# Optimization experiments

Hardware: AMD Instinct MI355X
Metric: run time of the kernel (lower is better)

The kernel has to match this reference:

```python
import jax, jax.numpy as jnp
import numpy as np
from jax import lax

T, D_IN, D_OUT = 8192, 4096, 4096
N_ADAPT, RANK = 8, 16


def setup_inputs() -> dict:
    key = jax.random.key(0)
    ks = jax.random.split(key, 6)
    x = jax.random.normal(ks[0], (T, D_IN), jnp.float32)
    weight_indices = jax.random.randint(ks[1], (T,), 0, N_ADAPT, jnp.int64 if jax.config.jax_enable_x64 else jnp.int32)
    W_base = jax.random.normal(ks[2], (D_OUT, D_IN), jnp.float32) * 0.02
    A_buffer = jax.random.normal(ks[3], (N_ADAPT, D_IN, RANK), jnp.float32) * 0.02
    B_buffer = jax.random.normal(ks[4], (N_ADAPT, RANK, D_OUT), jnp.float32) * 0.02
    DeltaW = jax.random.normal(ks[5], (N_ADAPT, D_IN, D_OUT), jnp.float32) * 0.02
    return {"x": x, "weight_indices": weight_indices, "W_base": W_base,
            "A_buffer": A_buffer, "B_buffer": B_buffer, "DeltaW": DeltaW}


def _ldmm(indices, x, A, B, D):
    """Per-token adapter matmul: out[t] = x[t] @ (DeltaW[j] + A[j] @ B[j]), j = indices[t].
    Grouped by adapter via masked GEMMs (fixed small adapter count), jit-friendly."""
    n_adapt = A.shape[0]
    acc0 = jnp.zeros((x.shape[0], D.shape[2]), x.dtype)

    def body(acc, inp):
        a_id, A_a, B_a, D_a = inp
        mask = (indices == a_id)[:, None]
        xm = jnp.where(mask, x, jnp.zeros((), x.dtype))  # [T, in]
        W_eff = D_a + A_a @ B_a                          # [in, out]
        return acc + xm @ W_eff, None

    acc, _ = lax.scan(body, acc0, (jnp.arange(n_adapt), A, B, D))
    return acc


def reference(x, weight_indices, W_base, A_buffer, B_buffer, DeltaW):
    base = x @ W_base.T                                   # ColumnParallelLinear
    delta = _ldmm(weight_indices, x, A_buffer, B_buffer, DeltaW)
    # NOTE: source has `base_output = +output` (unary plus, likely a typo for `+=`);
    # we implement the intended fused semantics base + ldmm.
    return base + delta
```

## Files before the change

### kernel.cpp

```cpp
#include <hip/hip_runtime.h>


#define T_TOKENS 8192
#define DIM 4096
#define NADAPT 8
#define RANK 16

#define BM2 256
#define MAXT2 40
#define GRIDX2 (MAXT2 * 16)

#define BM1 128
#define MAXT1 72

typedef __attribute__((ext_vector_type(8))) short bf16x8;
typedef __attribute__((ext_vector_type(4))) float f32x4;

__device__ __forceinline__ unsigned short f2bf(float f) {
  union { float f; unsigned u; } v; v.f = f;
  unsigned r = v.u + 0x7FFFu + ((v.u >> 16) & 1u);
  return (unsigned short)(r >> 16);
}

__device__ __forceinline__ void gload_lds16(const void* g, void* l) {
  __builtin_amdgcn_global_load_lds(
      (const __attribute__((address_space(1))) void*)g,
      (__attribute__((address_space(3))) void*)l, 16, 0, 0);
}

template <int N> __device__ __forceinline__ void vmwait() {
  if constexpr (N == 0)      asm volatile("s_waitcnt vmcnt(0)" ::: "memory");
  else if constexpr (N == 4) asm volatile("s_waitcnt vmcnt(4)" ::: "memory");
  else if constexpr (N == 8) asm volatile("s_waitcnt vmcnt(8)" ::: "memory");
}

__global__ void prep_kernel(const int* __restrict__ idx, int* __restrict__ perm,
                            int* __restrict__ meta, int padm) {
  __shared__ int s_cnt[NADAPT];
  __shared__ int s_padoff[NADAPT + 1];
  __shared__ int s_wsum[16];
  const int tid = threadIdx.x;
  const int lane = tid & 63;
  const int wave = tid >> 6;

  if (tid < NADAPT) s_cnt[tid] = 0;
  __syncthreads();
  for (int t = tid; t < T_TOKENS; t += 1024) atomicAdd(&s_cnt[idx[t]], 1);
  __syncthreads();

  if (tid == 0) {
    int off = 0, nt = 0;
    for (int j = 0; j < NADAPT; ++j) {
      meta[j] = s_cnt[j];
      s_padoff[j] = off;
      const int c = s_cnt[j];
      const int ntj = (c + padm - 1) / padm;
      for (int i = 0; i < ntj; ++i) {
        meta[32 + 3 * nt + 0] = j;
        meta[32 + 3 * nt + 1] = off + i * padm;
        meta[32 + 3 * nt + 2] = min(padm, c - i * padm);
        ++nt;
      }
      off += ntj * padm;
    }
    s_padoff[NADAPT] = off;
    meta[17] = nt;
    for (int j = 0; j <= NADAPT; ++j) meta[8 + j] = s_padoff[j];
  }
  __syncthreads();

  const int total_pad = s_padoff[NADAPT];
  for (int t = tid; t < total_pad; t += 1024) perm[t] = -1;
  __syncthreads();

  for (int j = 0; j < NADAPT; ++j) {
    int base = s_padoff[j];
    for (int c0 = 0; c0 < T_TOKENS; c0 += 1024) {
      const int t = c0 + tid;
      const int flag = (idx[t] == j) ? 1 : 0;
      const unsigned long long bal = __ballot(flag);
      const int wpos = __popcll(bal & ((1ULL << lane) - 1ULL));
      if (lane == 0) s_wsum[wave] = __popcll(bal);
      __syncthreads();
      int woff = 0, ctot = 0;
      for (int w = 0; w < 16; ++w) {
        const int v = s_wsum[w];
        if (w < wave) woff += v;
        ctot += v;
      }
      if (flag) perm[base + woff + wpos] = t;
      base += ctot;
      __syncthreads();
    }
  }
}

__global__ void convert_x_kernel(const float* __restrict__ x,
                                 unsigned short* __restrict__ xb) {
  const long long i = (long long)blockIdx.x * 256 + threadIdx.x;
  const float4* x4 = (const float4*)x;
  const float4 a = x4[2 * i];
  const float4 b = x4[2 * i + 1];
  uint4 o;
  o.x = (unsigned)f2bf(a.x) | ((unsigned)f2bf(a.y) << 16);
  o.y = (unsigned)f2bf(a.z) | ((unsigned)f2bf(a.w) << 16);
  o.z = (unsigned)f2bf(b.x) | ((unsigned)f2bf(b.y) << 16);
  o.w = (unsigned)f2bf(b.z) | ((unsigned)f2bf(b.w) << 16);
  ((uint4*)xb)[i] = o;
}

__global__ __launch_bounds__(256) void build_wtot_kernel(
    const float* __restrict__ Wb, const float* __restrict__ Am,
    const float* __restrict__ Bm, const float* __restrict__ DW,
    unsigned short* __restrict__ Wt, int j0) {
  const int jj = blockIdx.z;
  const int j = j0 + jj;
  const int i0 = blockIdx.x << 6;
  const int o0 = blockIdx.y << 6;
  __shared__ float Dl[64 * 64];
  __shared__ float Alt[16][68];
  __shared__ float Bl[16][68];
  const int tid = threadIdx.x;

  const float* dwp = DW + ((size_t)j * DIM + i0) * DIM + o0;
#pragma unroll
  for (int q = 0; q < 4; ++q) {
    const int lin = q * 256 + tid;
    const int i = lin >> 4;
    const int o4 = (lin & 15) << 2;
    const float4 v = *(const float4*)(dwp + (size_t)i * DIM + o4);
    const int iq = i >> 2, ie = i & 3;
#pragma unroll
    for (int k = 0; k < 4; ++k) {
      const int o = o4 + k;
      Dl[o * 64 + (((iq ^ (o & 15)) << 2) | ie)] = ((const float*)&v)[k];
    }
  }
  {
    const int ai = tid >> 2, r4 = (tid & 3) << 2;
    const float4 v = *(const float4*)(Am + ((size_t)j * DIM + i0 + ai) * RANK + r4);
#pragma unroll
    for (int k = 0; k < 4; ++k) Alt[r4 + k][ai] = ((const float*)&v)[k];
  }
  {
    const int br = tid >> 4, bo4 = (tid & 15) << 2;
    const float4 v = *(const float4*)(Bm + ((size_t)j * RANK + br) * DIM + o0 + bo4);
    *(float4*)&Bl[br][bo4] = v;
  }
  __syncthreads();

  const int to = (tid >> 4) << 2;
  const int ti = (tid & 15) << 2;
  float acc[4][4];

#pragma unroll
  for (int m = 0; m < 4; ++m) {
    const int o = to + m;
    const float4 w = *(const float4*)(Wb + (size_t)(o0 + o) * DIM + i0 + ti);
    const float4 d = *(const float4*)&Dl[o * 64 + (((ti >> 2) ^ (o & 15)) << 2)];
    acc[m][0] = w.x + d.x; acc[m][1] = w.y + d.y;
    acc[m][2] = w.z + d.z; acc[m][3] = w.w + d.w;
  }
#pragma unroll
  for (int r = 0; r < RANK; ++r) {
    const float4 av = *(const float4*)&Alt[r][ti];
    const float4 bv = *(const float4*)&Bl[r][to];
#pragma unroll
    for (int m = 0; m < 4; ++m) {
      const float b = ((const float*)&bv)[m];
      acc[m][0] += b * av.x; acc[m][1] += b * av.y;
      acc[m][2] += b * av.z; acc[m][3] += b * av.w;
    }
  }
#pragma unroll
  for (int m = 0; m < 4; ++m) {
    const int o = to + m;
    const unsigned lo = (unsigned)f2bf(acc[m][0]) | ((unsigned)f2bf(acc[m][1]) << 16);
    const unsigned hi = (unsigned)f2bf(acc[m][2]) | ((unsigned)f2bf(acc[m][3]) << 16);
    uint2 pk; pk.x = lo; pk.y = hi;
    *(uint2*)(Wt + ((size_t)jj * DIM + o0 + o) * DIM + i0 + ti) = pk;
  }
}

template <int BUF, int KK, int MQ, int VME, int SGRP, int SOP, int SKH, bool DOST>
__device__ __forceinline__ void do_phase(
    char* smem, int tid, int stile,
    const unsigned short* const* aB, const unsigned short* const* bB,
    const int* aoff, const int* boff, bf16x8* bfr, f32x4 (*acc)[4]) {
  const int grp = (BUF * 2 + KK) * 16384;
  if constexpr (MQ == 0) {
#pragma unroll
    for (int n = 0; n < 4; ++n)
      bfr[n] = *(const bf16x8*)(smem + 65536 + grp + boff[n]);
  }
  bf16x8 afr[4];
#pragma unroll
  for (int i = 0; i < 4; ++i)
    afr[i] = *(const bf16x8*)(smem + grp + aoff[MQ * 4 + i]);
  if constexpr (DOST) {
    const unsigned short* const* bs = SOP ? bB : aB;
#pragma unroll
    for (int q = 0; q < 2; ++q)
      gload_lds16(bs[q] + stile * 64 + SKH * 32,
                  smem + SOP * 65536 + SGRP * 16384 + q * 8192 + tid * 16);
  }
  __builtin_amdgcn_s_barrier();
  asm volatile("s_waitcnt lgkmcnt(0)" ::: "memory");
  __builtin_amdgcn_s_setprio(1);
#pragma unroll
  for (int i = 0; i < 4; ++i)
#pragma unroll
    for (int n = 0; n < 4; ++n)
      acc[MQ * 4 + i][n] =
          __builtin_amdgcn_mfma_f32_16x16x32_bf16(afr[i], bfr[n], acc[MQ * 4 + i][n], 0, 0, 0);
  __builtin_amdgcn_s_setprio(0);
  vmwait<VME>();
  __builtin_amdgcn_s_barrier();
}

template <int SGRP, int SOP, int SKH>
__device__ __forceinline__ void do_stage(
    char* smem, int tid, int stile,
    const unsigned short* const* aB, const unsigned short* const* bB) {
  const unsigned short* const* bs = SOP ? bB : aB;
#pragma unroll
  for (int q = 0; q < 2; ++q)
    gload_lds16(bs[q] + stile * 64 + SKH * 32,
                smem + SOP * 65536 + SGRP * 16384 + q * 8192 + tid * 16);
}

__global__ __launch_bounds__(512, 2) void gemm8_kernel(
    const unsigned short* __restrict__ xb, const unsigned short* __restrict__ Wt,
    const int* __restrict__ perm, const int* __restrict__ meta,
    float* __restrict__ out, int j0, int npp) {
  extern __shared__ char smem[];
  const int ntiles = meta[17];
  const int flat = blockIdx.x;
  const int swz = (flat & 7) * (GRIDX2 / 8) + (flat >> 3);
  const int mt = swz >> 4;
  const int nt = swz & 15;
  if (mt >= ntiles) return;
  const int adapter = meta[32 + 3 * mt];
  if (adapter < j0 || adapter >= j0 + npp) return;
  const int slot = adapter - j0;
  const int pbase = meta[32 + 3 * mt + 1];
  const int nbase = nt << 8;

  const int tid = threadIdx.x;
  const int lane = tid & 63;
  const int wave = tid >> 6;
  const int wr = wave >> 2, wc = wave & 3;
  const int fr = lane & 15, kg = lane >> 4;

  int aoff[8], boff[4];
#pragma unroll
  for (int m = 0; m < 8; ++m) {
    const int row = wr * 128 + m * 16 + fr;
    const int r = row >> 1, hf = row & 1;
    const int c = ((hf << 2) | kg) ^ (r & 7);
    aoff[m] = r * 128 + c * 16;
  }
#pragma unroll
  for (int n = 0; n < 4; ++n) {
    const int row = wc * 64 + n * 16 + fr;
    const int r = row >> 1, hf = row & 1;
    const int c = ((hf << 2) | kg) ^ (r & 7);
    boff[n] = r * 128 + c * 16;
  }

  const unsigned short* aB[2];
  const unsigned short* bB[2];
#pragma unroll
  for (int q = 0; q < 2; ++q) {
    const int L = q * 512 + tid;
    const int r = L >> 3, c = L & 7;
    const int s = c ^ (r & 7);
    const int grow = 2 * r + (s >> 2);
    const int gk = (s & 3) << 3;
    int pr = perm[pbase + grow];
    if (pr < 0) pr = 0;
    aB[q] = xb + (size_t)pr * DIM + gk;
    bB[q] = Wt + ((size_t)slot * DIM + nbase + grow) * DIM + gk;
  }

  const f32x4 zero = {0.f, 0.f, 0.f, 0.f};
  f32x4 acc[8][4];
#pragma unroll
  for (int m = 0; m < 8; ++m)
#pragma unroll
    for (int n = 0; n < 4; ++n) acc[m][n] = zero;
  bf16x8 bfr[4];

  do_stage<0, 0, 0>(smem, tid, 0, aB, bB);
  do_stage<0, 1, 0>(smem, tid, 0, aB, bB);
  do_stage<1, 0, 1>(smem, tid, 0, aB, bB);
  do_stage<1, 1, 1>(smem, tid, 0, aB, bB);
  do_stage<2, 0, 0>(smem, tid, 1, aB, bB);
  do_stage<2, 1, 0>(smem, tid, 1, aB, bB);
  vmwait<8>();
  __builtin_amdgcn_s_barrier();

  for (int it = 0; it < 31; ++it) {
    const int t1 = 2 * it + 1, t2 = 2 * it + 2, t3 = 2 * it + 3;
    do_phase<0, 0, 0, -1, 3, 0, 1, true>(smem, tid, t1, aB, bB, aoff, boff, bfr, acc);
    do_phase<0, 0, 1,  8, 3, 1, 1, true>(smem, tid, t1, aB, bB, aoff, boff, bfr, acc);
    do_phase<0, 1, 0, -1, 0, 0, 0, true>(smem, tid, t2, aB, bB, aoff, boff, bfr, acc);
    do_phase<0, 1, 1,  8, 0, 1, 0, true>(smem, tid, t2, aB, bB, aoff, boff, bfr, acc);
    do_phase<1, 0, 0, -1, 1, 0, 1, true>(smem, tid, t2, aB, bB, aoff, boff, bfr, acc);
    do_phase<1, 0, 1,  8, 1, 1, 1, true>(smem, tid, t2, aB, bB, aoff, boff, bfr, acc);
    do_phase<1, 1, 0, -1, 2, 0, 0, true>(smem, tid, t3, aB, bB, aoff, boff, bfr, acc);
    do_phase<1, 1, 1,  8, 2, 1, 0, true>(smem, tid, t3, aB, bB, aoff, boff, bfr, acc);
  }
  do_phase<0, 0, 0, -1, 3, 0, 1, true >(smem, tid, 63, aB, bB, aoff, boff, bfr, acc);
  do_phase<0, 0, 1,  8, 3, 1, 1, true >(smem, tid, 63, aB, bB, aoff, boff, bfr, acc);
  do_phase<0, 1, 0, -1, 0, 0, 0, false>(smem, tid, 0,  aB, bB, aoff, boff, bfr, acc);
  do_phase<0, 1, 1,  4, 0, 0, 0, false>(smem, tid, 0,  aB, bB, aoff, boff, bfr, acc);
  do_phase<1, 0, 0, -1, 0, 0, 0, false>(smem, tid, 0,  aB, bB, aoff, boff, bfr, acc);
  do_phase<1, 0, 1,  0, 0, 0, 0, false>(smem, tid, 0,  aB, bB, aoff, boff, bfr, acc);
  do_phase<1, 1, 0, -1, 0, 0, 0, false>(smem, tid, 0,  aB, bB, aoff, boff, bfr, acc);
  do_phase<1, 1, 1, -1, 0, 0, 0, false>(smem, tid, 0,  aB, bB, aoff, boff, bfr, acc);

#pragma unroll
  for (int m = 0; m < 8; ++m) {
#pragma unroll
    for (int t = 0; t < 4; ++t) {
      const int rt = wr * 128 + m * 16 + kg * 4 + t;
      const int pr = perm[pbase + rt];
      if (pr < 0) continue;
      float* orow = out + (size_t)pr * DIM + nbase + wc * 64;
#pragma unroll
      for (int n = 0; n < 4; ++n) orow[n * 16 + fr] = acc[m][n][t];
    }
  }
}

template <bool USE_XB>
__global__ __launch_bounds__(256) void gemm_kernel(
    const unsigned short* __restrict__ xb, const float* __restrict__ xf,
    const unsigned short* __restrict__ Wt,
    const int* __restrict__ perm, const int* __restrict__ meta,
    float* __restrict__ out, int j0, int npp) {
  const int ntiles = meta[17];
  const int mt = blockIdx.x;
  if (mt >= ntiles) return;
  const int adapter = meta[32 + 3 * mt];
  if (adapter < j0 || adapter >= j0 + npp) return;
  const int slot = adapter - j0;
  const int nt = blockIdx.y;
  const int pbase = meta[32 + 3 * mt + 1];
  const int nbase = nt << 7;

  __shared__ __align__(16) unsigned short As[BM1 * 64];
  __shared__ __align__(16) unsigned short Bs[BM1 * 64];

  const int tid = threadIdx.x;
  const int lane = tid & 63;
  const int wave = tid >> 6;

  const unsigned short* aSrcB[4];
  const float* aSrcF[4];
  const unsigned short* bSrc[4];
  unsigned short* aDst[4];
  unsigned short* bDst[4];
#pragma unroll
  for (int q = 0; q < 4; ++q) {
    const int c = wave * 4 + q;
    const int r = c * 8 + (lane >> 3);
    int pr = perm[pbase + r];
    if (pr < 0) pr = 0;
    if (USE_XB) aSrcB[q] = xb + (size_t)pr * DIM + (lane & 7) * 8;
    else        aSrcF[q] = xf + (size_t)pr * DIM + (lane & 7) * 8;
    bSrc[q] = Wt + ((size_t)slot * DIM + nbase + r) * DIM + (lane & 7) * 8;
    aDst[q] = As + c * 512;
    bDst[q] = Bs + c * 512;
  }

  const int wr = wave >> 1, wc = wave & 1;
  const int fr = lane & 15, kg = lane >> 4;

  const f32x4 zero = {0.f, 0.f, 0.f, 0.f};
  f32x4 acc[4][4];
#pragma unroll
  for (int m = 0; m < 4; ++m)
#pragma unroll
    for (int n = 0; n < 4; ++n) acc[m][n] = zero;

  for (int k0 = 0; k0 < DIM; k0 += 64) {
    if (USE_XB) {
#pragma unroll
      for (int q = 0; q < 4; ++q) gload_lds16(aSrcB[q] + k0, aDst[q]);
    } else {
#pragma unroll
      for (int q = 0; q < 4; ++q) {
        const float4 va = *(const float4*)(aSrcF[q] + k0);
        const float4 vb = *(const float4*)(aSrcF[q] + k0 + 4);
        union { bf16x8 v; unsigned short s[8]; } u;
        u.s[0] = f2bf(va.x); u.s[1] = f2bf(va.y); u.s[2] = f2bf(va.z); u.s[3] = f2bf(va.w);
        u.s[4] = f2bf(vb.x); u.s[5] = f2bf(vb.y); u.s[6] = f2bf(vb.z); u.s[7] = f2bf(vb.w);
        *(bf16x8*)(aDst[q] + lane * 8) = u.v;
      }
    }
#pragma unroll
    for (int q = 0; q < 4; ++q) gload_lds16(bSrc[q] + k0, bDst[q]);
    __syncthreads();
#pragma unroll
    for (int kk = 0; kk < 2; ++kk) {
      bf16x8 a[4], b[4];
#pragma unroll
      for (int m = 0; m < 4; ++m)
        a[m] = *(const bf16x8*)(&As[(wr * 64 + m * 16 + fr) * 64 + kk * 32 + kg * 8]);
#pragma unroll
      for (int n = 0; n < 4; ++n)
        b[n] = *(const bf16x8*)(&Bs[(wc * 64 + n * 16 + fr) * 64 + kk * 32 + kg * 8]);
#pragma unroll
      for (int m = 0; m < 4; ++m)
#pragma unroll
        for (int n = 0; n < 4; ++n)
          acc[m][n] = __builtin_amdgcn_mfma_f32_16x16x32_bf16(a[m], b[n], acc[m][n], 0, 0, 0);
    }
    __syncthreads();
  }

#pragma unroll
  for (int m = 0; m < 4; ++m) {
#pragma unroll
    for (int t = 0; t < 4; ++t) {
      const int rt = wr * 64 + m * 16 + kg * 4 + t;
      const int pr = perm[pbase + rt];
      if (pr < 0) continue;
      float* orow = out + (size_t)pr * DIM + nbase + wc * 64;
#pragma unroll
      for (int n = 0; n < 4; ++n) orow[n * 16 + fr] = acc[m][n][t];
    }
  }
}

extern "C" void kernel_launch(void* const* d_in, const int* in_sizes, int n_in,
                              void* d_out, int out_size, void* d_ws, size_t ws_size,
                              hipStream_t stream) {
  const float* x  = (const float*)d_in[0];
  const int* widx = (const int*)d_in[1];
  const float* Wb = (const float*)d_in[2];
  const float* Am = (const float*)d_in[3];
  const float* Bm = (const float*)d_in[4];
  const float* DW = (const float*)d_in[5];
  float* out = (float*)d_out;

  const size_t XB_BYTES = (size_t)T_TOKENS * DIM * 2;
  const size_t WT1_BYTES = (size_t)DIM * DIM * 2;
  const size_t PM_BYTES = 16384 * sizeof(int) + 4096;

  int npp = 0;
  bool use_xb = true;
  for (int cand = NADAPT; cand >= 1; cand >>= 1) {
    if (XB_BYTES + (size_t)cand * WT1_BYTES + PM_BYTES <= ws_size) { npp = cand; break; }
  }
  if (npp == 0) { npp = 1; use_xb = false; }

  bool use8 = use_xb &&
      (hipFuncSetAttribute((const void*)gemm8_kernel,
                           hipFuncAttributeMaxDynamicSharedMemorySize, 131072) == hipSuccess);

  char* ws = (char*)d_ws;
  unsigned short* xb = (unsigned short*)ws;
  unsigned short* Wt = (unsigned short*)(ws + (use_xb ? XB_BYTES : 0));
  char* tail = (char*)Wt + (size_t)npp * WT1_BYTES;
  int* perm = (int*)tail;
  int* meta = (int*)(tail + 16384 * sizeof(int));

  prep_kernel<<<dim3(1), dim3(1024), 0, stream>>>(widx, perm, meta, use8 ? BM2 : BM1);
  if (use_xb)
    convert_x_kernel<<<dim3(T_TOKENS * DIM / (256 * 8)), dim3(256), 0, stream>>>(x, xb);

  const int passes = NADAPT / npp;
  for (int p = 0; p < passes; ++p) {
    const int j0 = p * npp;
    build_wtot_kernel<<<dim3(DIM / 64, DIM / 64, npp), dim3(256), 0, stream>>>(
        Wb, Am, Bm, DW, Wt, j0);
    if (use8)
      gemm8_kernel<<<dim3(GRIDX2), dim3(512), 131072, stream>>>(
          xb, Wt, perm, meta, out, j0, npp);
    else if (use_xb)
      gemm_kernel<true><<<dim3(MAXT1, DIM / 128), dim3(256), 0, stream>>>(
          xb, nullptr, Wt, perm, meta, out, j0, npp);
    else
      gemm_kernel<false><<<dim3(MAXT1, DIM / 128), dim3(256), 0, stream>>>(
          nullptr, x, Wt, perm, meta, out, j0, npp);
  }
}
```

Before: 701.7 us.

## Build all adapter weights in one kernel reusing W_base tile with double-buffered prefetch

Adds a build kernel where each block loads its W_base tile once into registers and loops over all eight adapters. It double-buffers the DeltaW, A and B tiles in shared memory, prefetching the next adapter's data while computing the current one. This avoids re-reading W_base per adapter and overlaps global loads with compute. The old multi-pass path is kept only for when the workspace cannot hold all adapters. The new kernel doubles shared memory use and launches eight times fewer blocks, each doing more serial work.

```diff
diff --git a/kernel.cpp b/kernel.cpp
--- a/kernel.cpp
+++ b/kernel.cpp
@@ -109,6 +109,110 @@
   ((uint4*)xb)[i] = o;
 }
 
+__global__ __launch_bounds__(256) void build_wtot_all_kernel(
+    const float* __restrict__ Wb, const float* __restrict__ Am,
+    const float* __restrict__ Bm, const float* __restrict__ DW,
+    unsigned short* __restrict__ Wt) {
+  const int i0 = blockIdx.x << 6;
+  const int o0 = blockIdx.y << 6;
+  __shared__ float Dl[2][64 * 64];
+  __shared__ float Alt[2][16][68];
+  __shared__ float Bl[2][16][68];
+  const int tid = threadIdx.x;
+  const int to = (tid >> 4) << 2;
+  const int ti = (tid & 15) << 2;
+
+  float4 wbr[4];
+#pragma unroll
+  for (int m = 0; m < 4; ++m)
+    wbr[m] = *(const float4*)(Wb + (size_t)(o0 + to + m) * DIM + i0 + ti);
+
+  const int di = tid >> 4;
+  const int do4 = (tid & 15) << 2;
+  const int ar_i = tid >> 2, ar_r4 = (tid & 3) << 2;
+  const int br_r = tid >> 4, br_o4 = (tid & 15) << 2;
+
+  float4 dwr[4], ar, brv;
+  {
+    const float* dwp = DW + (size_t)i0 * DIM + o0;
+#pragma unroll
+    for (int q = 0; q < 4; ++q)
+      dwr[q] = *(const float4*)(dwp + (size_t)(q * 16 + di) * DIM + do4);
+    ar = *(const float4*)(Am + ((size_t)(i0 + ar_i)) * RANK + ar_r4);
+    brv = *(const float4*)(Bm + (size_t)br_r * DIM + o0 + br_o4);
+  }
+#pragma unroll
+  for (int q = 0; q < 4; ++q) {
+    const int i = q * 16 + di;
+    const int iq = i >> 2, ie = i & 3;
+#pragma unroll
+    for (int k = 0; k < 4; ++k) {
+      const int o = do4 + k;
+      Dl[0][o * 64 + (((iq ^ (o & 15)) << 2) | ie)] = ((const float*)&dwr[q])[k];
+    }
+  }
+#pragma unroll
+  for (int k = 0; k < 4; ++k) Alt[0][ar_r4 + k][ar_i] = ((const float*)&ar)[k];
+  *(float4*)&Bl[0][br_r][br_o4] = brv;
+  __syncthreads();
+
+  for (int j = 0; j < NADAPT; ++j) {
+    const int pb = j & 1;
+    if (j + 1 < NADAPT) {
+      const float* dwp = DW + ((size_t)(j + 1) * DIM + i0) * DIM + o0;
+#pragma unroll
+      for (int q = 0; q < 4; ++q)
+        dwr[q] = *(const float4*)(dwp + (size_t)(q * 16 + di) * DIM + do4);
+      ar = *(const float4*)(Am + ((size_t)(j + 1) * DIM + i0 + ar_i) * RANK + ar_r4);
+      brv = *(const float4*)(Bm + ((size_t)(j + 1) * RANK + br_r) * DIM + o0 + br_o4);
+    }
+    float acc[4][4];
+#pragma unroll
+    for (int m = 0; m < 4; ++m) {
+      const int o = to + m;
+      const float4 d = *(const float4*)&Dl[pb][o * 64 + (((ti >> 2) ^ (o & 15)) << 2)];
+      acc[m][0] = wbr[m].x + d.x; acc[m][1] = wbr[m].y + d.y;
+      acc[m][2] = wbr[m].z + d.z; acc[m][3] = wbr[m].w + d.w;
+    }
+#pragma unroll
+    for (int r = 0; r < RANK; ++r) {
+      const float4 av = *(const float4*)&Alt[pb][r][ti];
+      const float4 bv = *(const float4*)&Bl[pb][r][to];
+#pragma unroll
+      for (int m = 0; m < 4; ++m) {
+        const float b = ((const float*)&bv)[m];
+        acc[m][0] += b * av.x; acc[m][1] += b * av.y;
+        acc[m][2] += b * av.z; acc[m][3] += b * av.w;
+      }
+    }
+#pragma unroll
+    for (int m = 0; m < 4; ++m) {
+      const int o = to + m;
+      const unsigned lo = (unsigned)f2bf(acc[m][0]) | ((unsigned)f2bf(acc[m][1]) << 16);
+      const unsigned hi = (unsigned)f2bf(acc[m][2]) | ((unsigned)f2bf(acc[m][3]) << 16);
+      uint2 pk; pk.x = lo; pk.y = hi;
+      *(uint2*)(Wt + ((size_t)j * DIM + o0 + o) * DIM + i0 + ti) = pk;
+    }
+    if (j + 1 < NADAPT) {
+      const int nb = pb ^ 1;
+#pragma unroll
+      for (int q = 0; q < 4; ++q) {
+        const int i = q * 16 + di;
+        const int iq = i >> 2, ie = i & 3;
+#pragma unroll
+        for (int k = 0; k < 4; ++k) {
+          const int o = do4 + k;
+          Dl[nb][o * 64 + (((iq ^ (o & 15)) << 2) | ie)] = ((const float*)&dwr[q])[k];
+        }
+      }
+#pragma unroll
+      for (int k = 0; k < 4; ++k) Alt[nb][ar_r4 + k][ar_i] = ((const float*)&ar)[k];
+      *(float4*)&Bl[nb][br_r][br_o4] = brv;
+      __syncthreads();
+    }
+  }
+}
+
 __global__ __launch_bounds__(256) void build_wtot_kernel(
     const float* __restrict__ Wb, const float* __restrict__ Am,
     const float* __restrict__ Bm, const float* __restrict__ DW,
@@ -472,19 +576,27 @@
   if (use_xb)
     convert_x_kernel<<<dim3(T_TOKENS * DIM / (256 * 8)), dim3(256), 0, stream>>>(x, xb);
 
-  const int passes = NADAPT / npp;
-  for (int p = 0; p < passes; ++p) {
-    const int j0 = p * npp;
-    build_wtot_kernel<<<dim3(DIM / 64, DIM / 64, npp), dim3(256), 0, stream>>>(
-        Wb, Am, Bm, DW, Wt, j0);
+  if (npp == NADAPT) {
+    build_wtot_all_kernel<<<dim3(DIM / 64, DIM / 64), dim3(256), 0, stream>>>(
+        Wb, Am, Bm, DW, Wt);
     if (use8)
       gemm8_kernel<<<dim3(GRIDX2), dim3(512), 131072, stream>>>(
-          xb, Wt, perm, meta, out, j0, npp);
-    else if (use_xb)
+          xb, Wt, perm, meta, out, 0, NADAPT);
+    else
       gemm_kernel<true><<<dim3(MAXT1, DIM / 128), dim3(256), 0, stream>>>(
-          xb, nullptr, Wt, perm, meta, out, j0, npp);
-    else
-      gemm_kernel<false><<<dim3(MAXT1, DIM / 128), dim3(256), 0, stream>>>(
-          nullptr, x, Wt, perm, meta, out, j0, npp);
-  }
-}
+          xb, nullptr, Wt, perm, meta, out, 0, NADAPT);
+  } else {
+    const int passes = NADAPT / npp;
+    for (int p = 0; p < passes; ++p) {
+      const int j0 = p * npp;
+      build_wtot_kernel<<<dim3(DIM / 64, DIM / 64, npp), dim3(256), 0, stream>>>(
+          Wb, Am, Bm, DW, Wt, j0);
+      if (use_xb)
+        gemm_kernel<true><<<dim3(MAXT1, DIM / 128), dim3(256), 0, stream>>>(
+            xb, nullptr, Wt, perm, meta, out, j0, npp);
+      else
+        gemm_kernel<false><<<dim3(MAXT1, DIM / 128), dim3(256), 0, stream>>>(
+            nullptr, x, Wt, perm, meta, out, j0, npp);
+    }
+  }
+}
```

Result: faster. 642.7 us (-8.4%).
